# Performance work log

Hardware: AMD Instinct MI355X
Metric: run time of the kernel (lower is better)

Reference implementation:

```python
import jax, jax.numpy as jnp
import numpy as np

HIDDEN = 1024

def _init_linear(key, in_f, out_f):
    kw, kb = jax.random.split(key)
    bound = 1.0 / np.sqrt(in_f)
    W = jax.random.uniform(kw, (out_f, in_f), jnp.float32, -bound, bound)
    b = jax.random.uniform(kb, (out_f,), jnp.float32, -bound, bound)
    return W, b

def setup_inputs() -> dict:
    key = jax.random.key(0)
    ks = jax.random.split(key, 6)
    x = jax.random.normal(ks[0], (64, 512, 512), jnp.float32)
    # layer 0: input_size=512, hidden=1024
    W_rz0, b_rz0 = _init_linear(ks[1], 512 + HIDDEN, 2 * HIDDEN)
    W_n0, b_n0 = _init_linear(ks[2], 512 + HIDDEN, HIDDEN)
    # layer 1: input_size=hidden=1024
    W_rz1, b_rz1 = _init_linear(ks[3], HIDDEN + HIDDEN, 2 * HIDDEN)
    W_n1, b_n1 = _init_linear(ks[4], HIDDEN + HIDDEN, HIDDEN)
    # final fc: hidden -> output_size=512
    W_fc, b_fc = _init_linear(ks[5], HIDDEN, 512)
    return {"x": x, "W_rz0": W_rz0, "b_rz0": b_rz0, "W_n0": W_n0, "b_n0": b_n0,
            "W_rz1": W_rz1, "b_rz1": b_rz1, "W_n1": W_n1, "b_n1": b_n1,
            "W_fc": W_fc, "b_fc": b_fc}

def _gru_cell(xt, h, W_rz, b_rz, W_n, b_n):
    ih = jnp.concatenate([xt, h], axis=1)                 # [B, in+H]
    rz = ih @ W_rz.T + b_rz                               # [B, 2H]
    r, z = jnp.split(rz, 2, axis=1)
    r = jax.nn.sigmoid(r)
    z = jax.nn.sigmoid(z)
    ih_n = jnp.concatenate([xt, r * h], axis=1)
    n = jnp.tanh(ih_n @ W_n.T + b_n)
    return (1.0 - z) * n + z * h

def reference(x, W_rz0, b_rz0, W_n0, b_n0, W_rz1, b_rz1, W_n1, b_n1, W_fc, b_fc):
    B = x.shape[0]
    h0 = jnp.zeros((B, HIDDEN), x.dtype)
    h1 = jnp.zeros((B, HIDDEN), x.dtype)

    def step(carry, xt):
        h0, h1 = carry
        h0 = _gru_cell(xt, h0, W_rz0, b_rz0, W_n0, b_n0)
        h1 = _gru_cell(h0, h1, W_rz1, b_rz1, W_n1, b_n1)
        return (h0, h1), None

    xs = jnp.swapaxes(x, 0, 1)                            # [T, B, in]
    (h0, h1), _ = jax.lax.scan(step, (h0, h1), xs)
    # original returns outputs[:, -1, :] == fc(final hidden of last layer)
    return h1 @ W_fc.T + b_fc
```

## Files before the change

### kernel.cpp

```cpp
#include <hip/hip_runtime.h>
#include <math.h>

typedef _Float16 h8 __attribute__((ext_vector_type(8)));
typedef float f4 __attribute__((ext_vector_type(4)));

#define H 1024

#define OFF_WRZ0 0ull
#define OFF_WN0  6291456ull
#define OFF_WRZ1 9437184ull
#define OFF_WN1  17825792ull
#define OFF_H0BF 22020096ull
#define OFF_H1BF 22282240ull
#define OFF_RH0  22544384ull
#define OFF_RH1  22675456ull
#define OFF_H0F  22806528ull
#define OFF_H1F  23068672ull
#define OFF_Z0F  23330816ull
#define OFF_Z1F  23592960ull
#define OFF_CNT  23855104ull
#define ZERO_WORDS 458760

__device__ __forceinline__ unsigned long long llc_ld64(const void* p) {
  return __hip_atomic_load((const unsigned long long*)p, __ATOMIC_RELAXED, __HIP_MEMORY_SCOPE_AGENT);
}
__device__ __forceinline__ void llc_st64(void* p, unsigned long long v) {
  __hip_atomic_store((unsigned long long*)p, v, __ATOMIC_RELAXED, __HIP_MEMORY_SCOPE_AGENT);
}
__device__ __forceinline__ void llc_st32(void* p, unsigned v) {
  __hip_atomic_store((unsigned*)p, v, __ATOMIC_RELAXED, __HIP_MEMORY_SCOPE_AGENT);
}
__device__ __forceinline__ unsigned long long pack2f(float a, float b) {
  union { float f[2]; unsigned long long u; } x; x.f[0] = a; x.f[1] = b; return x.u;
}
__device__ __forceinline__ void unpack2f(unsigned long long v, float& a, float& b) {
  union { unsigned long long u; float f[2]; } x; x.u = v; a = x.f[0]; b = x.f[1];
}
__device__ __forceinline__ unsigned packh2(float a, float b) {
  union { _Float16 h[2]; unsigned u; } x; x.h[0] = (_Float16)a; x.h[1] = (_Float16)b; return x.u;
}

__global__ __launch_bounds__(256) void prep_kernel(
    const float* __restrict__ wrz0f, const float* __restrict__ wn0f,
    const float* __restrict__ wrz1f, const float* __restrict__ wn1f,
    _Float16* __restrict__ wrz0, _Float16* __restrict__ wn0,
    _Float16* __restrict__ wrz1, _Float16* __restrict__ wn1,
    unsigned* __restrict__ zbase) {
  size_t i = (size_t)blockIdx.x * blockDim.x + threadIdx.x;
  size_t stride = (size_t)gridDim.x * blockDim.x;
  for (size_t k = i; k < 2048ull * 1536ull; k += stride) wrz0[k] = (_Float16)wrz0f[k];
  for (size_t k = i; k < 1024ull * 1536ull; k += stride) wn0[k]  = (_Float16)wn0f[k];
  for (size_t k = i; k < 2048ull * 2048ull; k += stride) wrz1[k] = (_Float16)wrz1f[k];
  for (size_t k = i; k < 1024ull * 2048ull; k += stride) wn1[k]  = (_Float16)wn1f[k];
  for (size_t k = i; k < (size_t)ZERO_WORDS; k += stride) zbase[k] = 0u;
}

__device__ __forceinline__ void wait_ge(unsigned long long* c, unsigned long long tgt) {
  if (threadIdx.x == 0) {
    while (__hip_atomic_load(c, __ATOMIC_RELAXED, __HIP_MEMORY_SCOPE_AGENT) < tgt)
      __builtin_amdgcn_s_sleep(2);
  }
  __syncthreads();
}
__device__ __forceinline__ void signal(unsigned long long* c) {
  __syncthreads();
  if (threadIdx.x == 0)
    __hip_atomic_fetch_add(c, 1ull, __ATOMIC_RELAXED, __HIP_MEMORY_SCOPE_AGENT);
}

__device__ __forceinline__ void stage_chunk(const _Float16* __restrict__ src, int koff,
                                            _Float16* __restrict__ sA) {
  const int tid = threadIdx.x;
#pragma unroll
  for (int i = 0; i < 8; ++i) {
    int u = tid + (i << 10);
    int row = u >> 7;
    int c4 = (u & 127) << 2;
    unsigned long long v = llc_ld64(src + (size_t)row * H + koff + c4);
    unsigned byt = (((unsigned)row << 10) + ((unsigned)c4 << 1)) ^ (((unsigned)row & 7u) << 4);
    *(unsigned long long*)((char*)sA + byt) = v;
  }
}

template<int NT>
__device__ __forceinline__ void gemm_sA(const _Float16* __restrict__ sA,
                                        const _Float16* const* wps, int coff, f4* acc) {
  const int lane = threadIdx.x & 63;
  const int wv = threadIdx.x >> 6;
  const int kwq = wv & 3, mw = wv >> 2;
  const int rsub = lane & 15, kg = (lane >> 4) << 3;
  const int r = mw * 16 + rsub;
  const unsigned rb = ((unsigned)r << 10);
  const unsigned swz = ((unsigned)(r & 7) << 4);
#pragma unroll
  for (int k0 = 0; k0 < 128; k0 += 32) {
    int kc = kwq * 128 + k0 + kg;
    h8 a = *(const h8*)((const char*)sA + ((rb + ((unsigned)kc << 1)) ^ swz));
#pragma unroll
    for (int c = 0; c < NT; ++c) {
      h8 wf = *(const h8*)(wps[c] + coff + kc);
      acc[c] = __builtin_amdgcn_mfma_f32_16x16x32_f16(a, wf, acc[c], 0, 0, 0);
    }
  }
}

__device__ __forceinline__ void gemm_x(const float* __restrict__ x, int t,
                                       const _Float16* __restrict__ wr0,
                                       const _Float16* __restrict__ wr1,
                                       const _Float16* __restrict__ wn,
                                       f4* aRZ, f4* aN) {
  const int lane = threadIdx.x & 63;
  const int wv = threadIdx.x >> 6;
  const int kwq = wv & 3, mw = wv >> 2;
  const int rsub = lane & 15, kg = (lane >> 4) << 3;
  const float* xb = x + (size_t)(mw * 16 + rsub) * 262144 + (size_t)t * 512;
#pragma unroll
  for (int k0 = 0; k0 < 128; k0 += 32) {
    int k = kwq * 128 + k0 + kg;
    float4 f0 = *(const float4*)(xb + k);
    float4 f1 = *(const float4*)(xb + k + 4);
    h8 a;
    a[0] = (_Float16)f0.x; a[1] = (_Float16)f0.y; a[2] = (_Float16)f0.z; a[3] = (_Float16)f0.w;
    a[4] = (_Float16)f1.x; a[5] = (_Float16)f1.y; a[6] = (_Float16)f1.z; a[7] = (_Float16)f1.w;
    aRZ[0] = __builtin_amdgcn_mfma_f32_16x16x32_f16(a, *(const h8*)(wr0 + k), aRZ[0], 0, 0, 0);
    aRZ[1] = __builtin_amdgcn_mfma_f32_16x16x32_f16(a, *(const h8*)(wr1 + k), aRZ[1], 0, 0, 0);
    aN[0]  = __builtin_amdgcn_mfma_f32_16x16x32_f16(a, *(const h8*)(wn + k),  aN[0], 0, 0, 0);
  }
}

template<int NT>
__device__ __forceinline__ void red_write(float* __restrict__ red, const f4* acc) {
  const int lane = threadIdx.x & 63, wv = threadIdx.x >> 6;
  const int kwq = wv & 3, mw = wv >> 2;
  const int rsub = lane & 15, rg = lane >> 4;
#pragma unroll
  for (int c = 0; c < NT; ++c)
#pragma unroll
    for (int j = 0; j < 4; ++j)
      red[(size_t)(kwq * 64 + mw * 16 + rg * 4 + j) * 33 + c * 16 + rsub] = acc[c][j];
}

__device__ __forceinline__ void reduce_rz(const float* __restrict__ red, int cb,
    const float* __restrict__ bias, const float* __restrict__ hf,
    _Float16* __restrict__ rh, float* __restrict__ zf) {
  const int tid = threadIdx.x;
  const int row = tid >> 4, cp = (tid & 15) << 1;
  float v0 = 0.f, v1 = 0.f;
#pragma unroll
  for (int q = 0; q < 4; ++q) {
    const float* rr = red + (size_t)(q * 64 + row) * 33 + cp;
    v0 += rr[0]; v1 += rr[1];
  }
  v0 += bias[cb + cp]; v1 += bias[cb + cp + 1];
  float s0 = 1.f / (1.f + expf(-v0));
  float s1 = 1.f / (1.f + expf(-v1));
  if (cb < 1024) {
    float h0v, h1v;
    unpack2f(llc_ld64(hf + (size_t)row * H + cb + cp), h0v, h1v);
    llc_st32(rh + (size_t)row * H + cb + cp, packh2(s0 * h0v, s1 * h1v));
  } else {
    llc_st64(zf + (size_t)row * H + (cb - 1024) + cp, pack2f(s0, s1));
  }
}

__device__ __forceinline__ void reduce_n(const float* __restrict__ red, int nb,
    const float* __restrict__ bias, const float* __restrict__ zf,
    float* __restrict__ hf, _Float16* __restrict__ hb) {
  const int tid = threadIdx.x;
  if (tid < 512) {
    const int row = tid >> 3, cp = (tid & 7) << 1;
    float v0 = 0.f, v1 = 0.f;
#pragma unroll
    for (int q = 0; q < 4; ++q) {
      const float* rr = red + (size_t)(q * 64 + row) * 33 + cp;
      v0 += rr[0]; v1 += rr[1];
    }
    v0 += bias[nb + cp]; v1 += bias[nb + cp + 1];
    float n0 = tanhf(v0), n1 = tanhf(v1);
    float z0, z1, h0v, h1v;
    unpack2f(llc_ld64(zf + (size_t)row * H + nb + cp), z0, z1);
    unpack2f(llc_ld64(hf + (size_t)row * H + nb + cp), h0v, h1v);
    float o0 = (1.f - z0) * n0 + z0 * h0v;
    float o1 = (1.f - z1) * n1 + z1 * h1v;
    llc_st64(hf + (size_t)row * H + nb + cp, pack2f(o0, o1));
    llc_st32(hb + (size_t)row * H + nb + cp, packh2(o0, o1));
  }
}

__global__ __launch_bounds__(1024) void gru_main(const float* __restrict__ x,
    const _Float16* __restrict__ wrz0, const _Float16* __restrict__ wn0,
    const _Float16* __restrict__ wrz1, const _Float16* __restrict__ wn1,
    const float* __restrict__ brz0, const float* __restrict__ bn0,
    const float* __restrict__ brz1, const float* __restrict__ bn1,
    _Float16* __restrict__ h0bf, _Float16* __restrict__ h1bf,
    _Float16* __restrict__ rh0, _Float16* __restrict__ rh1,
    float* __restrict__ h0f, float* __restrict__ h1f,
    float* __restrict__ z0f, float* __restrict__ z1f,
    unsigned long long* __restrict__ cnt) {
  __shared__ char smem[65536];
  _Float16* sA = (_Float16*)smem;
  float* red = (float*)smem;
  const int bid = blockIdx.x;
  const int rsub = threadIdx.x & 15;

  if (bid < 64) {
    const int cb = bid * 32, nb = bid * 16;
    const _Float16* wpsRZ[2] = { wrz0 + (size_t)(cb + rsub) * 1536,
                                 wrz0 + (size_t)(cb + 16 + rsub) * 1536 };
    const _Float16* wpsN[1] = { wn0 + (size_t)(nb + rsub) * 1536 };
    for (int t = 0; t < 512; ++t) {
      f4 aRZ[2] = { f4{0.f,0.f,0.f,0.f}, f4{0.f,0.f,0.f,0.f} };
      f4 aN[1] = { f4{0.f,0.f,0.f,0.f} };
      gemm_x(x, t, wpsRZ[0], wpsRZ[1], wpsN[0], aRZ, aN);
      wait_ge(&cnt[1], 64ull * (unsigned long long)t);
      const _Float16* h0p = h0bf + (size_t)((t + 1) & 1) * 65536;
#pragma unroll
      for (int ch = 0; ch < 2; ++ch) {
        stage_chunk(h0p, ch * 512, sA);
        __syncthreads();
        gemm_sA<2>(sA, wpsRZ, 512 + ch * 512, aRZ);
        __syncthreads();
      }
      red_write<2>(red, aRZ);
      __syncthreads();
      reduce_rz(red, cb, brz0, h0f, rh0, z0f);
      signal(&cnt[0]);
      wait_ge(&cnt[0], 64ull * (unsigned long long)(t + 1));
      if (t >= 1) wait_ge(&cnt[3], 64ull * (unsigned long long)(t - 1));
#pragma unroll
      for (int ch = 0; ch < 2; ++ch) {
        stage_chunk(rh0, ch * 512, sA);
        __syncthreads();
        gemm_sA<1>(sA, wpsN, 512 + ch * 512, aN);
        __syncthreads();
      }
      red_write<1>(red, aN);
      __syncthreads();
      reduce_n(red, nb, bn0, z0f, h0f, h0bf + (size_t)(t & 1) * 65536);
      signal(&cnt[1]);
    }
  } else {
    const int b = bid - 64;
    const int cb = b * 32, nb = b * 16;
    const _Float16* wps3[3] = { wrz1 + (size_t)(cb + rsub) * 2048,
                                wrz1 + (size_t)(cb + 16 + rsub) * 2048,
                                wn1  + (size_t)(nb + rsub) * 2048 };
    for (int t = 1; t <= 512; ++t) {
      const int s = t - 1;
      f4 acc3[3] = { f4{0.f,0.f,0.f,0.f}, f4{0.f,0.f,0.f,0.f}, f4{0.f,0.f,0.f,0.f} };
      wait_ge(&cnt[3], 64ull * (unsigned long long)s);
      const _Float16* h1p = h1bf + (size_t)(t & 1) * 65536;
#pragma unroll
      for (int ch = 0; ch < 2; ++ch) {
        stage_chunk(h1p, ch * 512, sA);
        __syncthreads();
        gemm_sA<2>(sA, wps3, 1024 + ch * 512, acc3);
        __syncthreads();
      }
      wait_ge(&cnt[1], 64ull * (unsigned long long)t);
      const _Float16* h0p = h0bf + (size_t)((t + 1) & 1) * 65536;
#pragma unroll
      for (int ch = 0; ch < 2; ++ch) {
        stage_chunk(h0p, ch * 512, sA);
        __syncthreads();
        gemm_sA<3>(sA, wps3, ch * 512, acc3);
        __syncthreads();
      }
      red_write<2>(red, acc3);
      __syncthreads();
      reduce_rz(red, cb, brz1, h1f, rh1, z1f);
      signal(&cnt[2]);
      wait_ge(&cnt[2], 64ull * (unsigned long long)t);
#pragma unroll
      for (int ch = 0; ch < 2; ++ch) {
        stage_chunk(rh1, ch * 512, sA);
        __syncthreads();
        gemm_sA<1>(sA, wps3 + 2, 1024 + ch * 512, acc3 + 2);
        __syncthreads();
      }
      red_write<1>(red, acc3 + 2);
      __syncthreads();
      reduce_n(red, nb, bn1, z1f, h1f, h1bf + (size_t)(s & 1) * 65536);
      signal(&cnt[3]);
    }
  }
}

__global__ __launch_bounds__(256) void fc_kernel(const float* __restrict__ h1f,
                                                 const float* __restrict__ wfc,
                                                 const float* __restrict__ bfc,
                                                 float* __restrict__ out) {
  const int bid = blockIdx.x;
#pragma unroll
  for (int rep = 0; rep < 2; ++rep) {
    int local = threadIdx.x + rep * 256;
    int b = local >> 3;
    int o = bid * 8 + (local & 7);
    const float4* hp = (const float4*)(h1f + (size_t)b * 1024);
    const float4* wp = (const float4*)(wfc + (size_t)o * 1024);
    float s = 0.f;
#pragma unroll 4
    for (int i2 = 0; i2 < 256; ++i2) {
      float4 hv = hp[i2], wv = wp[i2];
      s += hv.x * wv.x + hv.y * wv.y + hv.z * wv.z + hv.w * wv.w;
    }
    out[(size_t)b * 512 + o] = s + bfc[o];
  }
}

extern "C" void kernel_launch(void* const* d_in, const int* in_sizes, int n_in,
                              void* d_out, int out_size, void* d_ws, size_t ws_size,
                              hipStream_t stream) {
  const float* x    = (const float*)d_in[0];
  const float* Wrz0 = (const float*)d_in[1];
  const float* brz0 = (const float*)d_in[2];
  const float* Wn0  = (const float*)d_in[3];
  const float* bn0  = (const float*)d_in[4];
  const float* Wrz1 = (const float*)d_in[5];
  const float* brz1 = (const float*)d_in[6];
  const float* Wn1  = (const float*)d_in[7];
  const float* bn1  = (const float*)d_in[8];
  const float* Wfc  = (const float*)d_in[9];
  const float* bfc  = (const float*)d_in[10];
  float* out = (float*)d_out;
  char* ws = (char*)d_ws;

  _Float16* wrz0h = (_Float16*)(ws + OFF_WRZ0);
  _Float16* wn0h  = (_Float16*)(ws + OFF_WN0);
  _Float16* wrz1h = (_Float16*)(ws + OFF_WRZ1);
  _Float16* wn1h  = (_Float16*)(ws + OFF_WN1);
  _Float16* h0bf  = (_Float16*)(ws + OFF_H0BF);
  _Float16* h1bf  = (_Float16*)(ws + OFF_H1BF);
  _Float16* rh0   = (_Float16*)(ws + OFF_RH0);
  _Float16* rh1   = (_Float16*)(ws + OFF_RH1);
  float* h0f = (float*)(ws + OFF_H0F);
  float* h1f = (float*)(ws + OFF_H1F);
  float* z0f = (float*)(ws + OFF_Z0F);
  float* z1f = (float*)(ws + OFF_Z1F);
  unsigned long long* cnt = (unsigned long long*)(ws + OFF_CNT);

  prep_kernel<<<2048, 256, 0, stream>>>(Wrz0, Wn0, Wrz1, Wn1,
                                        wrz0h, wn0h, wrz1h, wn1h,
                                        (unsigned*)(ws + OFF_H0BF));
  gru_main<<<128, 1024, 0, stream>>>(x, wrz0h, wn0h, wrz1h, wn1h,
                                     brz0, bn0, brz1, bn1,
                                     h0bf, h1bf, rh0, rh1,
                                     h0f, h1f, z0f, z1f, cnt);
  fc_kernel<<<64, 256, 0, stream>>>(h1f, Wfc, bfc, out);
}
```

Baseline: 22.19 ms.

## Replicate hidden state per XCD cooperatively instead of per-block LDS staging

Each block now discovers its XCD id at startup and ranks itself among co-resident blocks. Instead of every block staging the full hidden/rh tensors from LLC into LDS in chunks, the blocks on an XCD cooperatively copy each tensor into a per-XCD replica, sync on a per-XCD counter, invalidate L1, and then read A operands straight from that L2-resident copy. It also skips the GEMM against all-zero initial states at t=0. This is meant to cut redundant cross-XCD traffic and LDS staging barriers, at the cost of extra per-XCD barriers and complex counter bookkeeping that could deadlock or race if the counts are wrong.

```diff
diff --git a/kernel.cpp b/kernel.cpp
--- a/kernel.cpp
+++ b/kernel.cpp
@@ -19,7 +19,11 @@
 #define OFF_Z0F  23330816ull
 #define OFF_Z1F  23592960ull
 #define OFF_CNT  23855104ull
-#define ZERO_WORDS 458760
+#define OFF_INFO 23855168ull
+#define OFF_CCNT 23855680ull
+#define OFF_CP   23859200ull
+#define CP_XCD_STRIDE 1048576ull
+#define ZERO_WORDS 458960
 
 __device__ __forceinline__ unsigned long long llc_ld64(const void* p) {
   return __hip_atomic_load((const unsigned long long*)p, __ATOMIC_RELAXED, __HIP_MEMORY_SCOPE_AGENT);
@@ -68,37 +72,39 @@
     __hip_atomic_fetch_add(c, 1ull, __ATOMIC_RELAXED, __HIP_MEMORY_SCOPE_AGENT);
 }
 
-__device__ __forceinline__ void stage_chunk(const _Float16* __restrict__ src, int koff,
-                                            _Float16* __restrict__ sA) {
-  const int tid = threadIdx.x;
-#pragma unroll
-  for (int i = 0; i < 8; ++i) {
-    int u = tid + (i << 10);
-    int row = u >> 7;
-    int c4 = (u & 127) << 2;
-    unsigned long long v = llc_ld64(src + (size_t)row * H + koff + c4);
-    unsigned byt = (((unsigned)row << 10) + ((unsigned)c4 << 1)) ^ (((unsigned)row & 7u) << 4);
-    *(unsigned long long*)((char*)sA + byt) = v;
-  }
+__device__ __forceinline__ void copy_tensor(const void* __restrict__ master,
+                                            void* __restrict__ cp,
+                                            int rank, int m,
+                                            unsigned long long* ccnt,
+                                            unsigned long long target) {
+  const unsigned long long* src = (const unsigned long long*)master;
+  unsigned long long* dst = (unsigned long long*)cp;
+  for (int u = rank * 1024 + (int)threadIdx.x; u < 16384; u += m * 1024)
+    dst[u] = llc_ld64(src + u);
+  __syncthreads();
+  if (threadIdx.x == 0) {
+    __hip_atomic_fetch_add(ccnt, 1ull, __ATOMIC_RELAXED, __HIP_MEMORY_SCOPE_AGENT);
+    while (__hip_atomic_load(ccnt, __ATOMIC_RELAXED, __HIP_MEMORY_SCOPE_AGENT) < target)
+      __builtin_amdgcn_s_sleep(2);
+  }
+  __syncthreads();
+  asm volatile("buffer_inv sc0" ::: "memory");
 }
 
 template<int NT>
-__device__ __forceinline__ void gemm_sA(const _Float16* __restrict__ sA,
+__device__ __forceinline__ void gemm_cp(const _Float16* __restrict__ A,
                                         const _Float16* const* wps, int coff, f4* acc) {
-  const int lane = threadIdx.x & 63;
-  const int wv = threadIdx.x >> 6;
+  const int lane = threadIdx.x & 63, wv = threadIdx.x >> 6;
   const int kwq = wv & 3, mw = wv >> 2;
   const int rsub = lane & 15, kg = (lane >> 4) << 3;
-  const int r = mw * 16 + rsub;
-  const unsigned rb = ((unsigned)r << 10);
-  const unsigned swz = ((unsigned)(r & 7) << 4);
-#pragma unroll
-  for (int k0 = 0; k0 < 128; k0 += 32) {
-    int kc = kwq * 128 + k0 + kg;
-    h8 a = *(const h8*)((const char*)sA + ((rb + ((unsigned)kc << 1)) ^ swz));
+  const _Float16* ap = A + (size_t)(mw * 16 + rsub) * 1024 + kwq * 256 + kg;
+#pragma unroll
+  for (int k0 = 0; k0 < 256; k0 += 32) {
+    h8 a = *(const h8*)(ap + k0);
+    int kc = coff + kwq * 256 + k0 + kg;
 #pragma unroll
     for (int c = 0; c < NT; ++c) {
-      h8 wf = *(const h8*)(wps[c] + coff + kc);
+      h8 wf = *(const h8*)(wps[c] + kc);
       acc[c] = __builtin_amdgcn_mfma_f32_16x16x32_f16(a, wf, acc[c], 0, 0, 0);
     }
   }
@@ -109,8 +115,7 @@
                                        const _Float16* __restrict__ wr1,
                                        const _Float16* __restrict__ wn,
                                        f4* aRZ, f4* aN) {
-  const int lane = threadIdx.x & 63;
-  const int wv = threadIdx.x >> 6;
+  const int lane = threadIdx.x & 63, wv = threadIdx.x >> 6;
   const int kwq = wv & 3, mw = wv >> 2;
   const int rsub = lane & 15, kg = (lane >> 4) << 3;
   const float* xb = x + (size_t)(mw * 16 + rsub) * 262144 + (size_t)t * 512;
@@ -196,14 +201,48 @@
     _Float16* __restrict__ rh0, _Float16* __restrict__ rh1,
     float* __restrict__ h0f, float* __restrict__ h1f,
     float* __restrict__ z0f, float* __restrict__ z1f,
-    unsigned long long* __restrict__ cnt) {
-  __shared__ char smem[65536];
-  _Float16* sA = (_Float16*)smem;
-  float* red = (float*)smem;
+    unsigned long long* __restrict__ cnt, unsigned* __restrict__ info,
+    unsigned long long* __restrict__ ccnt_all, char* __restrict__ cpbase) {
+  __shared__ float red[256 * 33];
+  __shared__ int sh_meta[5];
   const int bid = blockIdx.x;
-  const int rsub = threadIdx.x & 15;
-
-  if (bid < 64) {
+  const int tid = threadIdx.x;
+  const int myrole = (bid < 64) ? 0 : 1;
+
+  if (tid == 0) {
+    unsigned xcc;
+    asm volatile("s_getreg_b32 %0, hwreg(HW_REG_XCC_ID)" : "=s"(xcc));
+    xcc &= 7u;
+    llc_st32(&info[bid], 0x80000000u | xcc);
+    asm volatile("s_waitcnt vmcnt(0)" ::: "memory");
+    __hip_atomic_fetch_add(&cnt[4], 1ull, __ATOMIC_RELAXED, __HIP_MEMORY_SCOPE_AGENT);
+    while (__hip_atomic_load(&cnt[4], __ATOMIC_RELAXED, __HIP_MEMORY_SCOPE_AGENT) < 128ull)
+      __builtin_amdgcn_s_sleep(2);
+    int rankA = 0, mA = 0, rankR = 0, mR = 0;
+    for (int b = 0; b < 128; ++b) {
+      unsigned v = (unsigned)__hip_atomic_load(&info[b], __ATOMIC_RELAXED, __HIP_MEMORY_SCOPE_AGENT);
+      if ((v & 7u) == xcc) {
+        int role = (b < 64) ? 0 : 1;
+        if (b < bid) rankA++;
+        mA++;
+        if (role == myrole) { if (b < bid) rankR++; mR++; }
+      }
+    }
+    sh_meta[0] = (int)xcc; sh_meta[1] = rankA; sh_meta[2] = mA;
+    sh_meta[3] = rankR; sh_meta[4] = mR;
+  }
+  __syncthreads();
+  const int xcd = sh_meta[0], rankA = sh_meta[1], mA = sh_meta[2];
+  const int rankR = sh_meta[3], mR = sh_meta[4];
+  unsigned long long* cc = ccnt_all + (size_t)xcd * 4;
+  char* cpx = cpbase + (size_t)xcd * CP_XCD_STRIDE;
+  _Float16* cpH0[2]  = {(_Float16*)(cpx + 0*131072), (_Float16*)(cpx + 1*131072)};
+  _Float16* cpRH0[2] = {(_Float16*)(cpx + 2*131072), (_Float16*)(cpx + 3*131072)};
+  _Float16* cpH1[2]  = {(_Float16*)(cpx + 4*131072), (_Float16*)(cpx + 5*131072)};
+  _Float16* cpRH1[2] = {(_Float16*)(cpx + 6*131072), (_Float16*)(cpx + 7*131072)};
+  const int rsub = tid & 15;
+
+  if (myrole == 0) {
     const int cb = bid * 32, nb = bid * 16;
     const _Float16* wpsRZ[2] = { wrz0 + (size_t)(cb + rsub) * 1536,
                                  wrz0 + (size_t)(cb + 16 + rsub) * 1536 };
@@ -213,13 +252,10 @@
       f4 aN[1] = { f4{0.f,0.f,0.f,0.f} };
       gemm_x(x, t, wpsRZ[0], wpsRZ[1], wpsN[0], aRZ, aN);
       wait_ge(&cnt[1], 64ull * (unsigned long long)t);
-      const _Float16* h0p = h0bf + (size_t)((t + 1) & 1) * 65536;
-#pragma unroll
-      for (int ch = 0; ch < 2; ++ch) {
-        stage_chunk(h0p, ch * 512, sA);
-        __syncthreads();
-        gemm_sA<2>(sA, wpsRZ, 512 + ch * 512, aRZ);
-        __syncthreads();
+      if (t >= 1) {
+        copy_tensor(h0bf + (size_t)((t - 1) & 1) * 65536, cpH0[(t - 1) & 1],
+                    rankA, mA, &cc[0], (unsigned long long)mA * t);
+        gemm_cp<2>(cpH0[(t - 1) & 1], wpsRZ, 512, aRZ);
       }
       red_write<2>(red, aRZ);
       __syncthreads();
@@ -227,12 +263,9 @@
       signal(&cnt[0]);
       wait_ge(&cnt[0], 64ull * (unsigned long long)(t + 1));
       if (t >= 1) wait_ge(&cnt[3], 64ull * (unsigned long long)(t - 1));
-#pragma unroll
-      for (int ch = 0; ch < 2; ++ch) {
-        stage_chunk(rh0, ch * 512, sA);
-        __syncthreads();
-        gemm_sA<1>(sA, wpsN, 512 + ch * 512, aN);
-        __syncthreads();
+      if (t >= 1) {
+        copy_tensor(rh0, cpRH0[t & 1], rankR, mR, &cc[1], (unsigned long long)mR * t);
+        gemm_cp<1>(cpRH0[t & 1], wpsN, 512, aN);
       }
       red_write<1>(red, aN);
       __syncthreads();
@@ -240,8 +273,7 @@
       signal(&cnt[1]);
     }
   } else {
-    const int b = bid - 64;
-    const int cb = b * 32, nb = b * 16;
+    const int b = bid - 64, cb = b * 32, nb = b * 16;
     const _Float16* wps3[3] = { wrz1 + (size_t)(cb + rsub) * 2048,
                                 wrz1 + (size_t)(cb + 16 + rsub) * 2048,
                                 wn1  + (size_t)(nb + rsub) * 2048 };
@@ -249,34 +281,29 @@
       const int s = t - 1;
       f4 acc3[3] = { f4{0.f,0.f,0.f,0.f}, f4{0.f,0.f,0.f,0.f}, f4{0.f,0.f,0.f,0.f} };
       wait_ge(&cnt[3], 64ull * (unsigned long long)s);
-      const _Float16* h1p = h1bf + (size_t)(t & 1) * 65536;
-#pragma unroll
-      for (int ch = 0; ch < 2; ++ch) {
-        stage_chunk(h1p, ch * 512, sA);
-        __syncthreads();
-        gemm_sA<2>(sA, wps3, 1024 + ch * 512, acc3);
-        __syncthreads();
+      if (s >= 1) {
+        copy_tensor(h1bf + (size_t)((s - 1) & 1) * 65536, cpH1[(s - 1) & 1],
+                    rankR, mR, &cc[2], (unsigned long long)mR * s);
+        gemm_cp<2>(cpH1[(s - 1) & 1], wps3, 1024, acc3);
       }
       wait_ge(&cnt[1], 64ull * (unsigned long long)t);
-      const _Float16* h0p = h0bf + (size_t)((t + 1) & 1) * 65536;
-#pragma unroll
-      for (int ch = 0; ch < 2; ++ch) {
-        stage_chunk(h0p, ch * 512, sA);
-        __syncthreads();
-        gemm_sA<3>(sA, wps3, ch * 512, acc3);
-        __syncthreads();
+      {
+        int rk = (t <= 511) ? rankA : rankR;
+        int mm = (t <= 511) ? mA : mR;
+        unsigned long long tg = (t <= 511) ? (unsigned long long)mA * t
+                                           : (unsigned long long)mA * 511 + (unsigned long long)mR;
+        copy_tensor(h0bf + (size_t)((t - 1) & 1) * 65536, cpH0[(t - 1) & 1],
+                    rk, mm, &cc[0], tg);
+        gemm_cp<3>(cpH0[(t - 1) & 1], wps3, 0, acc3);
       }
       red_write<2>(red, acc3);
       __syncthreads();
       reduce_rz(red, cb, brz1, h1f, rh1, z1f);
       signal(&cnt[2]);
       wait_ge(&cnt[2], 64ull * (unsigned long long)t);
-#pragma unroll
-      for (int ch = 0; ch < 2; ++ch) {
-        stage_chunk(rh1, ch * 512, sA);
-        __syncthreads();
-        gemm_sA<1>(sA, wps3 + 2, 1024 + ch * 512, acc3 + 2);
-        __syncthreads();
+      if (s >= 1) {
+        copy_tensor(rh1, cpRH1[s & 1], rankR, mR, &cc[3], (unsigned long long)mR * s);
+        gemm_cp<1>(cpRH1[s & 1], wps3 + 2, 1024, acc3 + 2);
       }
       red_write<1>(red, acc3 + 2);
       __syncthreads();
@@ -338,6 +365,9 @@
   float* z0f = (float*)(ws + OFF_Z0F);
   float* z1f = (float*)(ws + OFF_Z1F);
   unsigned long long* cnt = (unsigned long long*)(ws + OFF_CNT);
+  unsigned* info = (unsigned*)(ws + OFF_INFO);
+  unsigned long long* ccnt = (unsigned long long*)(ws + OFF_CCNT);
+  char* cpbase = ws + OFF_CP;
 
   prep_kernel<<<2048, 256, 0, stream>>>(Wrz0, Wn0, Wrz1, Wn1,
                                         wrz0h, wn0h, wrz1h, wn1h,
@@ -345,6 +375,7 @@
   gru_main<<<128, 1024, 0, stream>>>(x, wrz0h, wn0h, wrz1h, wn1h,
                                      brz0, bn0, brz1, bn1,
                                      h0bf, h1bf, rh0, rh1,
-                                     h0f, h1f, z0f, z1f, cnt);
+                                     h0f, h1f, z0f, z1f,
+                                     cnt, info, ccnt, cpbase);
   fc_kernel<<<64, 256, 0, stream>>>(h1f, Wfc, bfc, out);
 }
```

New measurement: 22.82 ms. 1.03x slower.
